# Optimization experiments

Hardware: AMD Instinct MI355X
Metric: run time of the kernel (lower is better)

The kernel has to match this reference:

```python
import jax, jax.numpy as jnp
import numpy as np

T, H, E, I = 2048, 2048, 8, 1408

def setup_inputs() -> dict:
    key = jax.random.key(0)
    k1, k2, k3, k4 = jax.random.split(key, 4)
    x = jax.random.normal(k1, (T, H), dtype=jnp.float32)
    gate_w = jax.random.normal(k2, (H, E), dtype=jnp.float32) * (1.0 / np.sqrt(H))
    w1 = jax.random.normal(k3, (E, H, I), dtype=jnp.float32) * (1.0 / np.sqrt(H))
    w2 = jax.random.normal(k4, (E, I, H), dtype=jnp.float32) * (1.0 / np.sqrt(I))
    return {"x": x, "gate_w": gate_w, "w1": w1, "w2": w2, "topk": 2}


def reference(x, gate_w, w1, w2, topk):
    # Router: logits -> softmax (fp32) -> top-k -> renormalize (fused_moe default)
    logits = x @ gate_w                                   # [T, E]
    probs = jax.nn.softmax(logits.astype(jnp.float32), axis=-1)
    tk_w, tk_i = jax.lax.top_k(probs, topk)               # [T, k]
    tk_w = tk_w / jnp.sum(tk_w, axis=-1, keepdims=True)
    # Scatter top-k weights into dense [T, E] combine matrix (zeros elsewhere)
    t_idx = jnp.arange(x.shape[0])[:, None]
    w_full = jnp.zeros(probs.shape, probs.dtype).at[t_idx, tk_i].set(tk_w)
    # Expert MLP: silu(x @ w1[e]) @ w2[e], combined with routing weights
    mid = jnp.einsum('th,ehi->tei', x, w1)                # [T, E, I]
    y = jnp.einsum('tei,eih->teh', jax.nn.silu(mid), w2)  # [T, E, H]
    out = jnp.einsum('te,teh->th', w_full.astype(x.dtype), y)
    return out
```

## Files before the change

### kernel.cpp

```cpp
#include <hip/hip_runtime.h>
#include <hip/hip_bf16.h>
#include <math.h>

#define TT 2048
#define HH 2048
#define EE 8
#define II 1408
#define PMAX 4608
#define MAXTILES 48
#define G1TILES (MAXTILES * (II / 64))
#define G2TILES (MAXTILES * (HH / 64))
#define NCONV 5632
#define ESPLIT 4

typedef short bf16x8 __attribute__((ext_vector_type(8)));
typedef float f32x4 __attribute__((ext_vector_type(4)));
typedef unsigned int u32;
typedef unsigned short u16;

__device__ __forceinline__ u16 f2bf(float f) {
  union { float f; u32 u; } v; v.f = f;
  u32 r = v.u + 0x7fffu + ((v.u >> 16) & 1u);
  return (u16)(r >> 16);
}

__device__ __forceinline__ float bf2f(u16 b) {
  union { u32 u; float f; } v; v.u = ((u32)b) << 16; return v.f;
}

__device__ __forceinline__ void gload16(const void* g, void* l) {
  __builtin_amdgcn_global_load_lds((const __attribute__((address_space(1))) u32*)g,
                                   (__attribute__((address_space(3))) u32*)l, 16, 0, 0);
}

__device__ __forceinline__ void conv_block(const float* __restrict__ w, u16* __restrict__ wb,
                                           int K, int N, int b, u16* smem) {
  int nx = N / 64, ky = K / 64;
  int n0 = (b % nx) * 64;
  int k0 = ((b / nx) % ky) * 64;
  int e  = b / (nx * ky);
  u16 (*sT)[76] = (u16(*)[76])smem;
  const float* we = w + (size_t)e * K * N;
  u16* wbe = wb + (size_t)e * K * N;
  int tid = threadIdx.x;
  int kl = tid >> 4, n4 = tid & 15;
#pragma unroll
  for (int j = 0; j < 4; ++j) {
    int k = kl + j * 16;
    float4 v = *(const float4*)(we + (size_t)(k0 + k) * N + n0 + n4 * 4);
    sT[n4 * 4 + 0][k] = f2bf(v.x);
    sT[n4 * 4 + 1][k] = f2bf(v.y);
    sT[n4 * 4 + 2][k] = f2bf(v.z);
    sT[n4 * 4 + 3][k] = f2bf(v.w);
  }
  __syncthreads();
  int nl = tid >> 3, kc = tid & 7;
#pragma unroll
  for (int j = 0; j < 2; ++j) {
    int n = nl + j * 32;
    uint4 v = *(const uint4*)(&sT[n][kc * 8]);
    *(uint4*)(wbe + (size_t)(n0 + n) * K + k0 + kc * 8) = v;
  }
}

template <int KDIM, int MODE, int ELO, int EHI>
__device__ __forceinline__ void gemm128_body(int L, const u16* __restrict__ A,
                                             const u16* __restrict__ B,
                                             const int* __restrict__ t_row0,
                                             const int* __restrict__ t_e,
                                             const int* __restrict__ t_rlim,
                                             u16* __restrict__ outp, u16* smem) {
  constexpr int Ndim = (MODE == 2) ? HH : II;
  constexpr int NCB = Ndim / 64;
  constexpr int NT = KDIM / 64;

  int xcd = L & 7;
  int q = L >> 3;
  int g = q / NCB;
  int n0b = q - g * NCB;
  int ti = g * 8 + xcd;
  int row0 = t_row0[ti];
  if (row0 < 0) return;
  int e = t_e[ti];
  if (e < ELO || e >= EHI) return;
  int rlim = t_rlim[ti];
  int n0 = n0b * 64;

  u16 (*sA)[64] = (u16(*)[64])smem;
  u16 (*sB)[64] = (u16(*)[64])(smem + 8192);

  int tid = threadIdx.x;
  int lane = tid & 63, wv = tid >> 6;
  int wm = wv >> 1, wn = wv & 1;
  int fr = lane & 15, kg = lane >> 4;

  int rA = lane >> 3;
  int colsw = ((lane & 7) ^ rA) * 8;
  const u16* Abase = A + (size_t)(row0 + rA) * KDIM + colsw;
  const u16* Bbase = B + (size_t)e * (size_t)Ndim * KDIM + (size_t)(n0 + rA) * KDIM + colsw;

  f32x4 acc[4][2];
#pragma unroll
  for (int m = 0; m < 4; ++m)
#pragma unroll
    for (int n = 0; n < 2; ++n)
      acc[m][n] = (f32x4){0.f, 0.f, 0.f, 0.f};

  for (int t = 0; t < NT; ++t) {
    int kof = t * 64;
#pragma unroll
    for (int j = 0; j < 4; ++j) {
      int c = wv * 4 + j;
      gload16(Abase + (size_t)c * 8 * KDIM + kof, &sA[c * 8][0]);
    }
#pragma unroll
    for (int j = 0; j < 2; ++j) {
      int c = wv * 2 + j;
      gload16(Bbase + (size_t)c * 8 * KDIM + kof, &sB[c * 8][0]);
    }
    __syncthreads();
#pragma unroll
    for (int kh = 0; kh < 2; ++kh) {
      bf16x8 af[4], bg[2];
      int cbyte = (kh * 64 + kg * 16) ^ ((fr & 7) << 4);
#pragma unroll
      for (int m = 0; m < 4; ++m)
        af[m] = *(const bf16x8*)((const char*)&sA[0][0] + (wm * 64 + m * 16 + fr) * 128 + cbyte);
#pragma unroll
      for (int n = 0; n < 2; ++n)
        bg[n] = *(const bf16x8*)((const char*)&sB[0][0] + (wn * 32 + n * 16 + fr) * 128 + cbyte);
#pragma unroll
      for (int m = 0; m < 4; ++m)
#pragma unroll
        for (int n = 0; n < 2; ++n)
          acc[m][n] = __builtin_amdgcn_mfma_f32_16x16x32_bf16(af[m], bg[n], acc[m][n], 0, 0, 0);
    }
    __syncthreads();
  }

#pragma unroll
  for (int m = 0; m < 4; ++m) {
    int lr = wm * 64 + m * 16 + kg * 4;
#pragma unroll
    for (int n = 0; n < 2; ++n) {
      int lc = wn * 32 + n * 16 + fr;
#pragma unroll
      for (int r = 0; r < 4; ++r) {
        int rr = row0 + lr + r;
        if (rr < rlim) {
          if constexpr (MODE == 0) {
            float v = acc[m][n][r];
            float s = v / (1.f + expf(-v));
            outp[(size_t)rr * II + n0 + lc] = f2bf(s);
          } else {
            outp[(size_t)rr * HH + n0 + lc] = f2bf(acc[m][n][r]);
          }
        }
      }
    }
  }
}

__global__ void router_conv_kernel(const float* __restrict__ x, const float* __restrict__ gw,
                                   int* __restrict__ tk_id, float* __restrict__ tk_w,
                                   const float* __restrict__ w1, u16* __restrict__ w1b) {
  __shared__ u16 smem[64 * 76];
  if (blockIdx.x < TT / 4) {
    int wv = threadIdx.x >> 6, lane = threadIdx.x & 63;
    int t = blockIdx.x * 4 + wv;
    float acc[EE];
#pragma unroll
    for (int e = 0; e < EE; ++e) acc[e] = 0.f;
    const float* xr = x + (size_t)t * HH;
    for (int h = lane; h < HH; h += 64) {
      float xv = xr[h];
      const float* g = gw + (size_t)h * EE;
#pragma unroll
      for (int e = 0; e < EE; ++e) acc[e] += xv * g[e];
    }
#pragma unroll
    for (int off = 32; off > 0; off >>= 1) {
#pragma unroll
      for (int e = 0; e < EE; ++e) acc[e] += __shfl_down(acc[e], off, 64);
    }
    if (lane == 0) {
      int i0 = 0;
#pragma unroll
      for (int e = 1; e < EE; ++e) if (acc[e] > acc[i0]) i0 = e;
      int i1 = (i0 == 0) ? 1 : 0;
#pragma unroll
      for (int e = 0; e < EE; ++e) { if (e == i0) continue; if (acc[e] > acc[i1]) i1 = e; }
      float d = acc[i1] - acc[i0];
      float p1 = expf(d);
      float w0 = 1.f / (1.f + p1);
      float w1v = p1 * w0;
      tk_id[2 * t] = i0; tk_id[2 * t + 1] = i1;
      tk_w[2 * t] = w0;  tk_w[2 * t + 1] = w1v;
    }
  } else {
    conv_block(w1, w1b, HH, II, blockIdx.x - TT / 4, smem);
  }
}

__global__ void scanassign_kernel(const int* __restrict__ tk_id, const float* __restrict__ tk_w,
                                  int* __restrict__ offsets, int* __restrict__ poff,
                                  int* __restrict__ tok_list, float* __restrict__ wt_list,
                                  int* __restrict__ islot,
                                  int* __restrict__ t_row0, int* __restrict__ t_e,
                                  int* __restrict__ t_rlim) {
  __shared__ int s_cnt[EE];
  __shared__ int s_off[EE + 1];
  __shared__ int s_poff[EE + 1];
  __shared__ int s_cur[EE];
  int tid = threadIdx.x;
  if (tid < EE) { s_cnt[tid] = 0; s_cur[tid] = 0; }
  __syncthreads();
  for (int i = tid; i < 2 * TT; i += 256) atomicAdd(&s_cnt[tk_id[i]], 1);
  __syncthreads();
  if (tid == 0) {
    int s = 0, ps = 0;
    for (int e = 0; e < EE; ++e) {
      s_off[e] = s; s_poff[e] = ps;
      s += s_cnt[e];
      ps += ((s_cnt[e] + 63) >> 6) << 6;
    }
    s_off[EE] = s; s_poff[EE] = ps;
    for (int e = 0; e <= EE; ++e) { offsets[e] = s_off[e]; poff[e] = s_poff[e]; }
    int nt = 0;
    for (int e = 0; e < EE; ++e) {
      for (int r0 = s_poff[e]; r0 < s_poff[e + 1]; r0 += 128) {
        t_row0[nt] = r0; t_e[nt] = e; t_rlim[nt] = s_poff[e + 1]; ++nt;
      }
    }
    for (int i = nt; i < MAXTILES; ++i) t_row0[i] = -1;
  }
  __syncthreads();
  for (int t = tid; t < TT; t += 256) {
#pragma unroll
    for (int k = 0; k < 2; ++k) {
      int e = tk_id[2 * t + k];
      int p = atomicAdd(&s_cur[e], 1);
      tok_list[s_off[e] + p] = t;
      wt_list[s_off[e] + p] = tk_w[2 * t + k];
      islot[2 * t + k] = s_poff[e] + p;
    }
  }
}

__global__ void gather_x_kernel(const float* __restrict__ x, const int* __restrict__ tok_list,
                                const int* __restrict__ offsets, const int* __restrict__ poff,
                                u16* __restrict__ xg) {
  int p = blockIdx.x;
  if (p >= poff[EE]) return;
  int e = 0;
#pragma unroll
  for (int q = 1; q < EE; ++q) if (p >= poff[q]) e = q;
  int cnt = offsets[e + 1] - offsets[e];
  int r = p - poff[e]; if (r >= cnt) r = cnt - 1;
  int tok = tok_list[offsets[e] + r];
  int c = threadIdx.x * 8;
  float4 v0 = *(const float4*)(x + (size_t)tok * HH + c);
  float4 v1 = *(const float4*)(x + (size_t)tok * HH + c + 4);
  u16 o[8] = { f2bf(v0.x), f2bf(v0.y), f2bf(v0.z), f2bf(v0.w),
               f2bf(v1.x), f2bf(v1.y), f2bf(v1.z), f2bf(v1.w) };
  *(uint4*)(xg + (size_t)p * HH + c) = *(uint4*)o;
}

__global__ void k4a_kernel(const u16* __restrict__ xg, const u16* __restrict__ w1b,
                           const int* __restrict__ t_row0, const int* __restrict__ t_e,
                           const int* __restrict__ t_rlim, u16* __restrict__ midB,
                           const float* __restrict__ w2, u16* __restrict__ w2b) {
  __shared__ u16 smem[12288];
  if (blockIdx.x >= G1TILES) {
    conv_block(w2, w2b, II, HH, blockIdx.x - G1TILES, smem);
    return;
  }
  gemm128_body<HH, 0, 0, ESPLIT>(blockIdx.x, xg, w1b, t_row0, t_e, t_rlim, midB, smem);
}

__global__ void k4b_kernel(const u16* __restrict__ xg, const u16* __restrict__ w1b,
                           u16* __restrict__ midB, const u16* __restrict__ w2b,
                           u16* __restrict__ y,
                           const int* __restrict__ t_row0, const int* __restrict__ t_e,
                           const int* __restrict__ t_rlim) {
  __shared__ u16 smem[12288];
  if (blockIdx.x < G1TILES) {
    gemm128_body<HH, 0, ESPLIT, EE>(blockIdx.x, xg, w1b, t_row0, t_e, t_rlim, midB, smem);
  } else {
    gemm128_body<II, 2, 0, ESPLIT>(blockIdx.x - G1TILES, midB, w2b, t_row0, t_e, t_rlim, y, smem);
  }
}

__global__ void k5_kernel(const u16* __restrict__ midB, const u16* __restrict__ w2b,
                          u16* __restrict__ y,
                          const int* __restrict__ t_row0, const int* __restrict__ t_e,
                          const int* __restrict__ t_rlim) {
  __shared__ u16 smem[12288];
  gemm128_body<II, 2, ESPLIT, EE>(blockIdx.x, midB, w2b, t_row0, t_e, t_rlim, y, smem);
}

__global__ void combine_kernel(const u16* __restrict__ y, const int* __restrict__ islot,
                               const float* __restrict__ tk_w, float* __restrict__ out) {
  int t = blockIdx.x;
  int h = threadIdx.x * 8;
  int s0 = islot[2 * t], s1 = islot[2 * t + 1];
  float w0 = tk_w[2 * t], w1 = tk_w[2 * t + 1];
  uint4 a = *(const uint4*)(y + (size_t)s0 * HH + h);
  uint4 b = *(const uint4*)(y + (size_t)s1 * HH + h);
  const u16* ap = (const u16*)&a;
  const u16* bp = (const u16*)&b;
  float* op = out + (size_t)t * HH + h;
  float4 r0, r1;
  r0.x = w0 * bf2f(ap[0]) + w1 * bf2f(bp[0]);
  r0.y = w0 * bf2f(ap[1]) + w1 * bf2f(bp[1]);
  r0.z = w0 * bf2f(ap[2]) + w1 * bf2f(bp[2]);
  r0.w = w0 * bf2f(ap[3]) + w1 * bf2f(bp[3]);
  r1.x = w0 * bf2f(ap[4]) + w1 * bf2f(bp[4]);
  r1.y = w0 * bf2f(ap[5]) + w1 * bf2f(bp[5]);
  r1.z = w0 * bf2f(ap[6]) + w1 * bf2f(bp[6]);
  r1.w = w0 * bf2f(ap[7]) + w1 * bf2f(bp[7]);
  *(float4*)(op) = r0;
  *(float4*)(op + 4) = r1;
}

__global__ void zero_kernel(float4* __restrict__ out4, int n4) {
  int i = blockIdx.x * blockDim.x + threadIdx.x;
  int stride = gridDim.x * blockDim.x;
  float4 z; z.x = 0.f; z.y = 0.f; z.z = 0.f; z.w = 0.f;
  for (int j = i; j < n4; j += stride) out4[j] = z;
}

__global__ void router_kernel(const float* __restrict__ x, const float* __restrict__ gw,
                              int* __restrict__ tk_id, float* __restrict__ tk_w) {
  int t = blockIdx.x;
  int lane = threadIdx.x;
  float acc[EE];
#pragma unroll
  for (int e = 0; e < EE; ++e) acc[e] = 0.f;
  const float* xr = x + (size_t)t * HH;
  for (int h = lane; h < HH; h += 64) {
    float xv = xr[h];
    const float* g = gw + (size_t)h * EE;
#pragma unroll
    for (int e = 0; e < EE; ++e) acc[e] += xv * g[e];
  }
#pragma unroll
  for (int off = 32; off > 0; off >>= 1) {
#pragma unroll
    for (int e = 0; e < EE; ++e) acc[e] += __shfl_down(acc[e], off, 64);
  }
  if (lane == 0) {
    int i0 = 0;
#pragma unroll
    for (int e = 1; e < EE; ++e) if (acc[e] > acc[i0]) i0 = e;
    int i1 = (i0 == 0) ? 1 : 0;
#pragma unroll
    for (int e = 0; e < EE; ++e) { if (e == i0) continue; if (acc[e] > acc[i1]) i1 = e; }
    float d = acc[i1] - acc[i0];
    float p1 = expf(d);
    float w0 = 1.f / (1.f + p1);
    float w1v = p1 * w0;
    tk_id[2 * t] = i0; tk_id[2 * t + 1] = i1;
    tk_w[2 * t] = w0;  tk_w[2 * t + 1] = w1v;
  }
}

__launch_bounds__(256, 2)
__global__ void gemm1_small(const float* __restrict__ x, const float* __restrict__ w1,
                            const int* __restrict__ tok_list, const int* __restrict__ offsets,
                            u16* __restrict__ mid) {
  int e = blockIdx.z;
  int g_off = offsets[e];
  int n_e = offsets[e + 1] - g_off;
  int row0 = blockIdx.y * 64;
  if (row0 >= n_e) return;
  int n0 = blockIdx.x * 64;
  __shared__ u16 sA[64][72];
  __shared__ u16 sB[64][72];
  __shared__ int s_tok[64];
  int tid = threadIdx.x;
  if (tid < 64) {
    int r = row0 + tid;
    s_tok[tid] = tok_list[g_off + ((r < n_e) ? r : (n_e - 1))];
  }
  __syncthreads();
  int lane = tid & 63;
  int wv = tid >> 6;
  int wm = wv >> 1, wn = wv & 1;
  int fr = lane & 15, kg = lane >> 4;
  f32x4 acc[2][2];
#pragma unroll
  for (int i = 0; i < 2; ++i)
#pragma unroll
    for (int j = 0; j < 2; ++j) acc[i][j] = (f32x4){0.f, 0.f, 0.f, 0.f};
  const float* w1e = w1 + (size_t)e * HH * II;
  for (int k0 = 0; k0 < HH; k0 += 64) {
#pragma unroll
    for (int i = 0; i < 4; ++i) {
      int idx = tid + i * 256;
      int r = idx >> 4, c4 = idx & 15;
      float4 v = *(const float4*)(x + (size_t)s_tok[r] * HH + k0 + c4 * 4);
      unsigned long long pk = (unsigned long long)f2bf(v.x)
                            | ((unsigned long long)f2bf(v.y) << 16)
                            | ((unsigned long long)f2bf(v.z) << 32)
                            | ((unsigned long long)f2bf(v.w) << 48);
      *(unsigned long long*)(&sA[r][c4 * 4]) = pk;
    }
#pragma unroll
    for (int i = 0; i < 4; ++i) {
      int idx = tid + i * 256;
      int kk = idx >> 4, c4 = idx & 15;
      float4 v = *(const float4*)(w1e + (size_t)(k0 + kk) * II + n0 + c4 * 4);
      sB[c4 * 4 + 0][kk] = f2bf(v.x);
      sB[c4 * 4 + 1][kk] = f2bf(v.y);
      sB[c4 * 4 + 2][kk] = f2bf(v.z);
      sB[c4 * 4 + 3][kk] = f2bf(v.w);
    }
    __syncthreads();
#pragma unroll
    for (int kk = 0; kk < 64; kk += 32) {
      bf16x8 af[2], bg[2];
#pragma unroll
      for (int m = 0; m < 2; ++m) af[m] = *(const bf16x8*)(&sA[wm * 32 + m * 16 + fr][kk + kg * 8]);
#pragma unroll
      for (int n = 0; n < 2; ++n) bg[n] = *(const bf16x8*)(&sB[wn * 32 + n * 16 + fr][kk + kg * 8]);
#pragma unroll
      for (int m = 0; m < 2; ++m)
#pragma unroll
        for (int n = 0; n < 2; ++n)
          acc[m][n] = __builtin_amdgcn_mfma_f32_16x16x32_bf16(af[m], bg[n], acc[m][n], 0, 0, 0);
    }
    __syncthreads();
  }
#pragma unroll
  for (int m = 0; m < 2; ++m)
#pragma unroll
    for (int n = 0; n < 2; ++n)
#pragma unroll
      for (int r = 0; r < 4; ++r) {
        int lr = wm * 32 + m * 16 + kg * 4 + r;
        int lc = wn * 32 + n * 16 + fr;
        if (row0 + lr < n_e) {
          float v = acc[m][n][r];
          float s = v / (1.f + expf(-v));
          mid[(size_t)(g_off + row0 + lr) * II + n0 + lc] = f2bf(s);
        }
      }
}

__launch_bounds__(256, 2)
__global__ void gemm2_small(const u16* __restrict__ mid, const float* __restrict__ w2,
                            const int* __restrict__ tok_list, const float* __restrict__ wt_list,
                            const int* __restrict__ offsets, float* __restrict__ out) {
  int e = blockIdx.z;
  int g_off = offsets[e];
  int n_e = offsets[e + 1] - g_off;
  int row0 = blockIdx.y * 64;
  if (row0 >= n_e) return;
  int n0 = blockIdx.x * 64;
  __shared__ u16 sA[64][72];
  __shared__ u16 sB[64][72];
  __shared__ int s_tok[64];
  __shared__ float s_wt[64];
  int tid = threadIdx.x;
  if (tid < 64) {
    int r = row0 + tid;
    int cr = (r < n_e) ? r : (n_e - 1);
    s_tok[tid] = tok_list[g_off + cr];
    s_wt[tid] = wt_list[g_off + cr];
  }
  __syncthreads();
  int lane = tid & 63;
  int wv = tid >> 6;
  int wm = wv >> 1, wn = wv & 1;
  int fr = lane & 15, kg = lane >> 4;
  f32x4 acc[2][2];
#pragma unroll
  for (int i = 0; i < 2; ++i)
#pragma unroll
    for (int j = 0; j < 2; ++j) acc[i][j] = (f32x4){0.f, 0.f, 0.f, 0.f};
  const float* w2e = w2 + (size_t)e * II * HH;
  for (int k0 = 0; k0 < II; k0 += 64) {
#pragma unroll
    for (int i = 0; i < 2; ++i) {
      int idx = tid + i * 256;
      int r = idx >> 3, c8 = idx & 7;
      int gr = row0 + r; if (gr >= n_e) gr = n_e - 1;
      uint4 v = *(const uint4*)(mid + (size_t)(g_off + gr) * II + k0 + c8 * 8);
      *(uint4*)(&sA[r][c8 * 8]) = v;
    }
#pragma unroll
    for (int i = 0; i < 4; ++i) {
      int idx = tid + i * 256;
      int kk = idx >> 4, c4 = idx & 15;
      float4 v = *(const float4*)(w2e + (size_t)(k0 + kk) * HH + n0 + c4 * 4);
      sB[c4 * 4 + 0][kk] = f2bf(v.x);
      sB[c4 * 4 + 1][kk] = f2bf(v.y);
      sB[c4 * 4 + 2][kk] = f2bf(v.z);
      sB[c4 * 4 + 3][kk] = f2bf(v.w);
    }
    __syncthreads();
#pragma unroll
    for (int kk = 0; kk < 64; kk += 32) {
      bf16x8 af[2], bg[2];
#pragma unroll
      for (int m = 0; m < 2; ++m) af[m] = *(const bf16x8*)(&sA[wm * 32 + m * 16 + fr][kk + kg * 8]);
#pragma unroll
      for (int n = 0; n < 2; ++n) bg[n] = *(const bf16x8*)(&sB[wn * 32 + n * 16 + fr][kk + kg * 8]);
#pragma unroll
      for (int m = 0; m < 2; ++m)
#pragma unroll
        for (int n = 0; n < 2; ++n)
          acc[m][n] = __builtin_amdgcn_mfma_f32_16x16x32_bf16(af[m], bg[n], acc[m][n], 0, 0, 0);
    }
    __syncthreads();
  }
#pragma unroll
  for (int m = 0; m < 2; ++m)
#pragma unroll
    for (int n = 0; n < 2; ++n)
#pragma unroll
      for (int r = 0; r < 4; ++r) {
        int lr = wm * 32 + m * 16 + kg * 4 + r;
        int lc = wn * 32 + n * 16 + fr;
        if (row0 + lr < n_e) {
          float v = acc[m][n][r] * s_wt[lr];
          atomicAdd(out + (size_t)s_tok[lr] * HH + n0 + lc, v);
        }
      }
}

extern "C" void kernel_launch(void* const* d_in, const int* in_sizes, int n_in,
                              void* d_out, int out_size, void* d_ws, size_t ws_size,
                              hipStream_t stream) {
  const float* x  = (const float*)d_in[0];
  const float* gw = (const float*)d_in[1];
  const float* w1 = (const float*)d_in[2];
  const float* w2 = (const float*)d_in[3];
  float* out = (float*)d_out;

  char* ws = (char*)d_ws;
  int*   tk_id    = (int*)(ws);
  float* tk_w     = (float*)(ws + 16384);
  int*   offsets  = (int*)(ws + 32832);
  int*   poff     = (int*)(ws + 32896);
  int*   tok_list = (int*)(ws + 33024);
  float* wt_list  = (float*)(ws + 49408);
  int*   islot    = (int*)(ws + 65792);
  int*   t_row0   = (int*)(ws + 98304);
  int*   t_e      = (int*)(ws + 98560);
  int*   t_rlim   = (int*)(ws + 98816);

  u16* xg    = (u16*)(ws + (1u << 20));
  u16* midBp = (u16*)(ws + (20u << 20));
  u16* w1b   = (u16*)(ws + (33u << 20));
  u16* w2b   = (u16*)(ws + 80740352u);
  u16* y     = (u16*)(ws + (33u << 20));
  const size_t NEED = 126877696u;

  if (ws_size >= NEED) {
    router_conv_kernel<<<TT / 4 + NCONV, 256, 0, stream>>>(x, gw, tk_id, tk_w, w1, w1b);
    scanassign_kernel<<<1, 256, 0, stream>>>(tk_id, tk_w, offsets, poff, tok_list, wt_list,
                                             islot, t_row0, t_e, t_rlim);
    gather_x_kernel<<<PMAX, 256, 0, stream>>>(x, tok_list, offsets, poff, xg);
    k4a_kernel<<<G1TILES + NCONV, 256, 0, stream>>>(
        xg, w1b, t_row0, t_e, t_rlim, midBp, w2, w2b);
    k4b_kernel<<<G1TILES + G2TILES, 256, 0, stream>>>(
        xg, w1b, midBp, w2b, y, t_row0, t_e, t_rlim);
    k5_kernel<<<G2TILES, 256, 0, stream>>>(midBp, w2b, y, t_row0, t_e, t_rlim);
    combine_kernel<<<TT, 256, 0, stream>>>(y, islot, tk_w, out);
  } else {
    u16* mid0 = (u16*)(ws + 131072);
    router_kernel<<<TT, 64, 0, stream>>>(x, gw, tk_id, tk_w);
    scanassign_kernel<<<1, 256, 0, stream>>>(tk_id, tk_w, offsets, poff, tok_list, wt_list,
                                             islot, t_row0, t_e, t_rlim);
    zero_kernel<<<1024, 256, 0, stream>>>((float4*)out, TT * HH / 4);
    gemm1_small<<<dim3(II / 64, TT / 64, EE), 256, 0, stream>>>(x, w1, tok_list, offsets, mid0);
    gemm2_small<<<dim3(HH / 64, TT / 64, EE), 256, 0, stream>>>(mid0, w2, tok_list, wt_list, offsets, out);
  }
}
```

Measured before the change: 188.0 us.

## Replace expert-split staggered GEMM pipeline with plain GEMM1 then GEMM2 launches

```diff
diff --git a/kernel.cpp b/kernel.cpp
--- a/kernel.cpp
+++ b/kernel.cpp
@@ -9,9 +9,7 @@
 #define PMAX 4608
 #define MAXTILES 48
 #define G1TILES (MAXTILES * (II / 64))
-#define G2TILES (MAXTILES * (HH / 64))
 #define NCONV 5632
-#define ESPLIT 4
 
 typedef short bf16x8 __attribute__((ext_vector_type(8)));
 typedef float f32x4 __attribute__((ext_vector_type(4)));
@@ -63,7 +61,7 @@
   }
 }
 
-template <int KDIM, int MODE, int ELO, int EHI>
+template <int KDIM, int MODE>
 __device__ __forceinline__ void gemm128_body(int L, const u16* __restrict__ A,
                                              const u16* __restrict__ B,
                                              const int* __restrict__ t_row0,
@@ -82,7 +80,6 @@
   int row0 = t_row0[ti];
   if (row0 < 0) return;
   int e = t_e[ti];
-  if (e < ELO || e >= EHI) return;
   int rlim = t_rlim[ti];
   int n0 = n0b * 64;
 
@@ -266,37 +263,24 @@
   *(uint4*)(xg + (size_t)p * HH + c) = *(uint4*)o;
 }
 
-__global__ void k4a_kernel(const u16* __restrict__ xg, const u16* __restrict__ w1b,
-                           const int* __restrict__ t_row0, const int* __restrict__ t_e,
-                           const int* __restrict__ t_rlim, u16* __restrict__ midB,
-                           const float* __restrict__ w2, u16* __restrict__ w2b) {
+__global__ void gemm1_conv_kernel(const u16* __restrict__ xg, const u16* __restrict__ w1b,
+                                  const int* __restrict__ t_row0, const int* __restrict__ t_e,
+                                  const int* __restrict__ t_rlim, u16* __restrict__ midB,
+                                  const float* __restrict__ w2, u16* __restrict__ w2b) {
   __shared__ u16 smem[12288];
   if (blockIdx.x >= G1TILES) {
     conv_block(w2, w2b, II, HH, blockIdx.x - G1TILES, smem);
     return;
   }
-  gemm128_body<HH, 0, 0, ESPLIT>(blockIdx.x, xg, w1b, t_row0, t_e, t_rlim, midB, smem);
-}
-
-__global__ void k4b_kernel(const u16* __restrict__ xg, const u16* __restrict__ w1b,
-                           u16* __restrict__ midB, const u16* __restrict__ w2b,
-                           u16* __restrict__ y,
-                           const int* __restrict__ t_row0, const int* __restrict__ t_e,
-                           const int* __restrict__ t_rlim) {
+  gemm128_body<HH, 0>(blockIdx.x, xg, w1b, t_row0, t_e, t_rlim, midB, smem);
+}
+
+__global__ void gemm2_kernel(const u16* __restrict__ midB, const u16* __restrict__ w2b,
+                             u16* __restrict__ y,
+                             const int* __restrict__ t_row0, const int* __restrict__ t_e,
+                             const int* __restrict__ t_rlim) {
   __shared__ u16 smem[12288];
-  if (blockIdx.x < G1TILES) {
-    gemm128_body<HH, 0, ESPLIT, EE>(blockIdx.x, xg, w1b, t_row0, t_e, t_rlim, midB, smem);
-  } else {
-    gemm128_body<II, 2, 0, ESPLIT>(blockIdx.x - G1TILES, midB, w2b, t_row0, t_e, t_rlim, y, smem);
-  }
-}
-
-__global__ void k5_kernel(const u16* __restrict__ midB, const u16* __restrict__ w2b,
-                          u16* __restrict__ y,
-                          const int* __restrict__ t_row0, const int* __restrict__ t_e,
-                          const int* __restrict__ t_rlim) {
-  __shared__ u16 smem[12288];
-  gemm128_body<II, 2, ESPLIT, EE>(blockIdx.x, midB, w2b, t_row0, t_e, t_rlim, y, smem);
+  gemm128_body<II, 2>(blockIdx.x, midB, w2b, t_row0, t_e, t_rlim, y, smem);
 }
 
 __global__ void combine_kernel(const u16* __restrict__ y, const int* __restrict__ islot,
@@ -563,11 +547,10 @@
     scanassign_kernel<<<1, 256, 0, stream>>>(tk_id, tk_w, offsets, poff, tok_list, wt_list,
                                              islot, t_row0, t_e, t_rlim);
     gather_x_kernel<<<PMAX, 256, 0, stream>>>(x, tok_list, offsets, poff, xg);
-    k4a_kernel<<<G1TILES + NCONV, 256, 0, stream>>>(
+    gemm1_conv_kernel<<<G1TILES + NCONV, 256, 0, stream>>>(
         xg, w1b, t_row0, t_e, t_rlim, midBp, w2, w2b);
-    k4b_kernel<<<G1TILES + G2TILES, 256, 0, stream>>>(
-        xg, w1b, midBp, w2b, y, t_row0, t_e, t_rlim);
-    k5_kernel<<<G2TILES, 256, 0, stream>>>(midBp, w2b, y, t_row0, t_e, t_rlim);
+    gemm2_kernel<<<MAXTILES * (HH / 64), 256, 0, stream>>>(
+        midBp, w2b, y, t_row0, t_e, t_rlim);
     combine_kernel<<<TT, 256, 0, stream>>>(y, islot, tk_w, out);
   } else {
     u16* mid0 = (u16*)(ws + 131072);
```

Measured after the change: 173.0 us (median of 2 runs). 8.0% less time.
